# Performance work log

Hardware: AMD Instinct MI355X
Metric: run time of the kernel (lower is better)

## Reference

```python
import math
import jax, jax.numpy as jnp
import numpy as np

B, L, D_MODEL = 2, 2048, 1024
N_HEAD, HEAD_DIM = 16, 64
ATT_SCALE = 1.0  # divisor is sqrt(head_dim ** attention_scale)


def setup_inputs() -> dict:
    key = jax.random.key(0)
    ks = jax.random.split(key, 6)
    HD = N_HEAD * HEAD_DIM
    # Xavier-uniform style init for projection weights (stored as [in, out])
    def xavier(k, fan_in, fan_out):
        lim = math.sqrt(6.0 / (fan_in + fan_out))
        return jax.random.uniform(k, (fan_in, fan_out), jnp.float32, -lim, lim)
    return {
        "x":  jax.random.normal(ks[0], (B, L, D_MODEL), jnp.float32),
        "Wq": xavier(ks[1], D_MODEL, HD), "bq": jnp.zeros((HD,), jnp.float32),
        "Wk": xavier(ks[2], D_MODEL, HD), "bk": jnp.zeros((HD,), jnp.float32),
        "Wv": xavier(ks[3], D_MODEL, HD), "bv": jnp.zeros((HD,), jnp.float32),
        "Wo": xavier(ks[4], HD, D_MODEL),
        "bo": jax.random.uniform(ks[5], (D_MODEL,), jnp.float32, -1.0 / math.sqrt(HD), 1.0 / math.sqrt(HD)),
    }


def reference(x, Wq, bq, Wk, bk, Wv, bv, Wo, bo):
    b, l, _ = x.shape
    # QKV projections -> [B, L, H, Dh]
    q = (x @ Wq + bq).reshape(b, l, N_HEAD, HEAD_DIM)
    k = (x @ Wk + bk).reshape(b, l, N_HEAD, HEAD_DIM)
    v = (x @ Wv + bv).reshape(b, l, N_HEAD, HEAD_DIM)
    scale = 1.0 / math.sqrt(HEAD_DIM ** ATT_SCALE)
    # Unnormalized (no softmax) attention: (Q K^T / sqrt(Dh)) V
    scores = jnp.einsum("blhd,bmhd->bhlm", q, k) * scale  # [B,H,L,L]
    attn = jnp.einsum("bhlm,bmhd->blhd", scores, v)        # [B,L,H,Dh]
    out = attn.reshape(b, l, N_HEAD * HEAD_DIM) @ Wo + bo  # dispatcher
    return out
```

## Files before the change

kernel.cpp:

```cpp
#include <hip/hip_runtime.h>
#include <stdint.h>

#define B_ 2
#define L_ 2048
#define DM 1024
#define NH 16
#define DH 64
#define M_ (B_*L_)
#define NQKV 3072

typedef short short8 __attribute__((ext_vector_type(8)));
typedef float f32x4 __attribute__((ext_vector_type(4)));

__device__ __forceinline__ unsigned short f2b(float f) {
    union { float f; unsigned int u; } v; v.f = f;
    unsigned int u = v.u;
    return (unsigned short)((u + 0x7fffu + ((u >> 16) & 1u)) >> 16);
}

__device__ __forceinline__ void gld_lds16(const void* g, void* l) {
    __builtin_amdgcn_global_load_lds(
        (const __attribute__((address_space(1))) void*)g,
        (__attribute__((address_space(3))) void*)l, 16, 0, 0);
}

__global__ __launch_bounds__(256)
void setup_kernel(const float* __restrict__ x,
                  const float* __restrict__ Wq, const float* __restrict__ Wk,
                  const float* __restrict__ Wv, const float* __restrict__ Wo,
                  const float* __restrict__ bq, const float* __restrict__ bk,
                  const float* __restrict__ bv,
                  unsigned short* __restrict__ xb, unsigned short* __restrict__ WqkvT,
                  unsigned short* __restrict__ WoT, float* __restrict__ biasq,
                  float* __restrict__ KtV)
{
    __shared__ float tile[32][33];
    const int bid = blockIdx.x;
    const int t = threadIdx.x;

    if (bid < 2048) {
        int i = (bid * 256 + t) * 8;
        float4 a0 = *(const float4*)(x + i);
        float4 a1 = *(const float4*)(x + i + 4);
        uint4 p;
        p.x = (unsigned)f2b(a0.x) | ((unsigned)f2b(a0.y) << 16);
        p.y = (unsigned)f2b(a0.z) | ((unsigned)f2b(a0.w) << 16);
        p.z = (unsigned)f2b(a1.x) | ((unsigned)f2b(a1.y) << 16);
        p.w = (unsigned)f2b(a1.z) | ((unsigned)f2b(a1.w) << 16);
        *(uint4*)(xb + i) = p;
    } else if (bid < 2048 + 4096) {
        int wb = bid - 2048;
        int wi = wb >> 10;
        int tid = wb & 1023;
        const float* W = (wi == 0) ? Wq : (wi == 1) ? Wk : (wi == 2) ? Wv : Wo;
        unsigned short* dst = (wi < 3) ? (WqkvT + (size_t)wi * 1024 * 1024) : WoT;
        int n0 = (tid & 31) * 32, k0 = (tid >> 5) * 32;
        int r = t >> 3, c4 = (t & 7) << 2;
        float4 v = *(const float4*)(W + (size_t)(k0 + r) * DM + n0 + c4);
        tile[r][c4+0] = v.x; tile[r][c4+1] = v.y; tile[r][c4+2] = v.z; tile[r][c4+3] = v.w;
        __syncthreads();
        uint2 o;
        o.x = (unsigned)f2b(tile[c4+0][r]) | ((unsigned)f2b(tile[c4+1][r]) << 16);
        o.y = (unsigned)f2b(tile[c4+2][r]) | ((unsigned)f2b(tile[c4+3][r]) << 16);
        *(uint2*)(dst + (size_t)(n0 + r) * DM + k0 + c4) = o;
    } else if (bid < 2048 + 4096 + 12) {
        int i = (bid - 6144) * 256 + t;
        float v = (i < 1024) ? bq[i] : (i < 2048 ? bk[i - 1024] : bv[i - 2048]);
        biasq[i] = v;
    } else {
        int i = ((bid - 6156) * 256 + t) * 4;
        float4 z; z.x = z.y = z.z = z.w = 0.f;
        *(float4*)(KtV + i) = z;
    }
}

template<int BN, bool OUT_BF16, bool BATCHED_B>
__global__ __launch_bounds__(256)
void gemm_tn_kernel(const unsigned short* __restrict__ A, int lda,
                    const unsigned short* __restrict__ Bt,
                    const float* __restrict__ bias,
                    void* __restrict__ C,
                    int M, int N, int K)
{
    constexpr int BM = 128;
    constexpr int MI = (BN == 128) ? 4 : 2;
    constexpr int MJ = 4;
    __shared__ __align__(16) unsigned short As[BM * 32];
    __shared__ __align__(16) unsigned short Bs[BN * 32];

    const int t = threadIdx.x;
    const int w = t >> 6, lane = t & 63;
    const int quad = lane >> 4, l16 = lane & 15;
    const int wm = (BN == 128) ? (w >> 1) : w;
    const int wn = (BN == 128) ? (w & 1) : 0;
    const int m0 = blockIdx.y * BM, n0 = blockIdx.x * BN;

    if constexpr (BATCHED_B) Bt += (size_t)(m0 >> 11) * 1024 * 1024;

    f32x4 acc[MI][MJ];
    #pragma unroll
    for (int i = 0; i < MI; i++)
        #pragma unroll
        for (int j = 0; j < MJ; j++)
            #pragma unroll
            for (int r = 0; r < 4; r++) acc[i][j][r] = 0.f;

    const int srow = t >> 2;
    const int schunk = t & 3;

    for (int kk = 0; kk < K; kk += 32) {
        #pragma unroll
        for (int p = 0; p < 2; p++) {
            int row = p * 64 + srow;
            int g = schunk ^ ((row >> 1) & 3);
            gld_lds16(A + (size_t)(m0 + row) * lda + kk + g * 8,
                      (char*)As + p * 4096 + w * 1024);
        }
        #pragma unroll
        for (int p = 0; p < BN / 64; p++) {
            int row = p * 64 + srow;
            int g = schunk ^ ((row >> 1) & 3);
            gld_lds16(Bt + (size_t)(n0 + row) * K + kk + g * 8,
                      (char*)Bs + p * 4096 + w * 1024);
        }
        __syncthreads();

        short8 afr[MI], bfr[MJ];
        #pragma unroll
        for (int i = 0; i < MI; i++) {
            int am = wm * (MI * 16) + i * 16 + l16;
            afr[i] = *(const short8*)((const char*)As + am * 64 + ((quad ^ ((am >> 1) & 3)) << 4));
        }
        #pragma unroll
        for (int j = 0; j < MJ; j++) {
            int bn = wn * 64 + j * 16 + l16;
            bfr[j] = *(const short8*)((const char*)Bs + bn * 64 + ((quad ^ ((bn >> 1) & 3)) << 4));
        }
        #pragma unroll
        for (int i = 0; i < MI; i++)
            #pragma unroll
            for (int j = 0; j < MJ; j++)
                acc[i][j] = __builtin_amdgcn_mfma_f32_16x16x32_bf16(afr[i], bfr[j], acc[i][j], 0, 0, 0);
        __syncthreads();
    }

    #pragma unroll
    for (int j = 0; j < MJ; j++) {
        int col = n0 + wn * 64 + j * 16 + l16;
        float bv = bias[col];
        #pragma unroll
        for (int i = 0; i < MI; i++) {
            #pragma unroll
            for (int r = 0; r < 4; r++) {
                int row = m0 + wm * (MI * 16) + i * 16 + quad * 4 + r;
                float v = acc[i][j][r] + bv;
                if constexpr (OUT_BF16)
                    ((unsigned short*)C)[(size_t)row * N + col] = f2b(v);
                else
                    ((float*)C)[(size_t)row * N + col] = v;
            }
        }
    }
}


__global__ __launch_bounds__(256)
void ktv_mfma_kernel(const unsigned short* __restrict__ QKV, float* __restrict__ KtV)
{
    __shared__ __align__(16) unsigned short Ksl[64][40];
    __shared__ __align__(16) unsigned short Vsl[64][40];

    const int bh = blockIdx.x, chunk = blockIdx.y;
    const int b = bh >> 4, h = bh & 15;
    const int t = threadIdx.x;
    const int wave = t >> 6, lane = t & 63;
    const int quad = lane >> 4, l16 = lane & 15;
    const int lrow = t >> 3, c0 = (t & 7) << 3;

    f32x4 acc[4];
    #pragma unroll
    for (int i = 0; i < 4; i++)
        #pragma unroll
        for (int r = 0; r < 4; r++) acc[i][r] = 0.f;

    const size_t base0 = ((size_t)(b * L_ + chunk * 128)) * NQKV + (size_t)h * DH;
    for (int kk = 0; kk < 128; kk += 32) {
        size_t rb = base0 + (size_t)(kk + lrow) * NQKV + c0;
        uint4 kp = *(const uint4*)(QKV + rb + 1024);
        uint4 vp = *(const uint4*)(QKV + rb + 2048);
        Ksl[c0+0][lrow] = (unsigned short)(kp.x & 0xffff);
        Ksl[c0+1][lrow] = (unsigned short)(kp.x >> 16);
        Ksl[c0+2][lrow] = (unsigned short)(kp.y & 0xffff);
        Ksl[c0+3][lrow] = (unsigned short)(kp.y >> 16);
        Ksl[c0+4][lrow] = (unsigned short)(kp.z & 0xffff);
        Ksl[c0+5][lrow] = (unsigned short)(kp.z >> 16);
        Ksl[c0+6][lrow] = (unsigned short)(kp.w & 0xffff);
        Ksl[c0+7][lrow] = (unsigned short)(kp.w >> 16);
        Vsl[c0+0][lrow] = (unsigned short)(vp.x & 0xffff);
        Vsl[c0+1][lrow] = (unsigned short)(vp.x >> 16);
        Vsl[c0+2][lrow] = (unsigned short)(vp.y & 0xffff);
        Vsl[c0+3][lrow] = (unsigned short)(vp.y >> 16);
        Vsl[c0+4][lrow] = (unsigned short)(vp.z & 0xffff);
        Vsl[c0+5][lrow] = (unsigned short)(vp.z >> 16);
        Vsl[c0+6][lrow] = (unsigned short)(vp.w & 0xffff);
        Vsl[c0+7][lrow] = (unsigned short)(vp.w >> 16);
        __syncthreads();

        short8 af = *(const short8*)&Ksl[wave * 16 + l16][quad * 8];
        #pragma unroll
        for (int nt = 0; nt < 4; nt++) {
            short8 bfr = *(const short8*)&Vsl[nt * 16 + l16][quad * 8];
            acc[nt] = __builtin_amdgcn_mfma_f32_16x16x32_bf16(af, bfr, acc[nt], 0, 0, 0);
        }
        __syncthreads();
    }

    float* dst0 = KtV + (size_t)bh * 64 * 64;
    #pragma unroll
    for (int nt = 0; nt < 4; nt++) {
        int col = nt * 16 + l16;
        #pragma unroll
        for (int r = 0; r < 4; r++) {
            int row = wave * 16 + quad * 4 + r;
            atomicAdd(dst0 + row * 64 + col, acc[nt][r] * 0.125f);
        }
    }
}

__global__ __launch_bounds__(256)
void zmat_kernel(const unsigned short* __restrict__ WoT, const float* __restrict__ KtV,
                 unsigned short* __restrict__ ZT)
{
    __shared__ __align__(16) unsigned short Asl[64][72];
    __shared__ __align__(16) unsigned short Bsl[64][72];

    const int bh = blockIdx.x, nt0 = blockIdx.y;
    const int b = bh >> 4, h = bh & 15;
    const int t = threadIdx.x;
    const int wave = t >> 6, lane = t & 63;
    const int quad = lane >> 4, l16 = lane & 15;
    const int n0 = nt0 * 64;
    const int row = t >> 2, c0 = (t & 3) << 4;

    const unsigned short* ap = WoT + (size_t)(n0 + row) * DM + h * DH + c0;
    *(uint4*)&Asl[row][c0]     = *(const uint4*)ap;
    *(uint4*)&Asl[row][c0 + 8] = *(const uint4*)(ap + 8);

    const float* kp = KtV + ((size_t)bh * 64 + row) * 64 + c0;
    #pragma unroll
    for (int j = 0; j < 16; j++) Bsl[row][c0 + j] = f2b(kp[j]);
    __syncthreads();

    f32x4 acc[4];
    #pragma unroll
    for (int i = 0; i < 4; i++)
        #pragma unroll
        for (int r = 0; r < 4; r++) acc[i][r] = 0.f;

    #pragma unroll
    for (int ks = 0; ks < 2; ks++) {
        short8 af = *(const short8*)&Asl[wave * 16 + l16][ks * 32 + quad * 8];
        #pragma unroll
        for (int nt = 0; nt < 4; nt++) {
            short8 bfr = *(const short8*)&Bsl[nt * 16 + l16][ks * 32 + quad * 8];
            acc[nt] = __builtin_amdgcn_mfma_f32_16x16x32_bf16(af, bfr, acc[nt], 0, 0, 0);
        }
    }

    unsigned short* zb = ZT + (size_t)b * 1024 * 1024 + (size_t)h * DH;
    #pragma unroll
    for (int nt = 0; nt < 4; nt++) {
        int col = nt * 16 + l16;
        #pragma unroll
        for (int r = 0; r < 4; r++) {
            int zr = n0 + wave * 16 + quad * 4 + r;
            zb[(size_t)zr * 1024 + col] = f2b(acc[nt][r]);
        }
    }
}


extern "C" void kernel_launch(void* const* d_in, const int* in_sizes, int n_in,
                              void* d_out, int out_size, void* d_ws, size_t ws_size,
                              hipStream_t stream)
{
    const float* x  = (const float*)d_in[0];
    const float* Wq = (const float*)d_in[1];
    const float* bq = (const float*)d_in[2];
    const float* Wk = (const float*)d_in[3];
    const float* bk = (const float*)d_in[4];
    const float* Wv = (const float*)d_in[5];
    const float* bv = (const float*)d_in[6];
    const float* Wo = (const float*)d_in[7];
    const float* bo = (const float*)d_in[8];

    char* ws = (char*)d_ws;
    unsigned short* xb    = (unsigned short*)(ws);
    unsigned short* WqkvT = (unsigned short*)(ws + (size_t)8  * 1024 * 1024);
    unsigned short* WoT   = (unsigned short*)(ws + (size_t)14 * 1024 * 1024);
    float*          biasq = (float*)         (ws + (size_t)16 * 1024 * 1024);
    unsigned short* QKV   = (unsigned short*)(ws + (size_t)17 * 1024 * 1024);
    float*          KtV   = (float*)         (ws + (size_t)41 * 1024 * 1024);
    unsigned short* ZT    = xb;

    setup_kernel<<<6284, 256, 0, stream>>>(x, Wq, Wk, Wv, Wo, bq, bk, bv,
                                           xb, WqkvT, WoT, biasq, KtV);

    gemm_tn_kernel<128, true, false><<<dim3(NQKV / 128, M_ / 128), 256, 0, stream>>>(
        xb, DM, WqkvT, biasq, QKV, M_, NQKV, DM);

    ktv_mfma_kernel<<<dim3(B_ * NH, 16), 256, 0, stream>>>(QKV, KtV);

    zmat_kernel<<<dim3(B_ * NH, 16), 256, 0, stream>>>(WoT, KtV, ZT);

    gemm_tn_kernel<64, false, true><<<dim3(DM / 64, M_ / 128), 256, 0, stream>>>(
        QKV, NQKV, ZT, bo, d_out, M_, DM, DM);
}
```

Baseline: 164.8 us.

## Fuse K^T V reduction into QKV projection GEMM epilogue with interleaved K/V weights

Reorders the K and V weight columns so each 128-wide output tile of the QKV GEMM holds one head's K and V. The new fused kernel then computes that tile's K^T V partial product in its epilogue and atomically accumulates it, and only Q is written to global memory. This removes the separate ktv kernel and the write-then-reread of K and V, and the 1/8 scale is folded into Wk and bk. In exchange the epilogue gains extra LDS traffic, MFMA work and atomics, and the new mainloop uses direct global-to-LDS loads with a swizzled layout.

```diff
diff --git a/kernel.cpp b/kernel.cpp
--- a/kernel.cpp
+++ b/kernel.cpp
@@ -53,24 +53,215 @@
         int wi = wb >> 10;
         int tid = wb & 1023;
         const float* W = (wi == 0) ? Wq : (wi == 1) ? Wk : (wi == 2) ? Wv : Wo;
-        unsigned short* dst = (wi < 3) ? (WqkvT + (size_t)wi * 1024 * 1024) : WoT;
+        float s = (wi == 1) ? 0.125f : 1.0f;
         int n0 = (tid & 31) * 32, k0 = (tid >> 5) * 32;
         int r = t >> 3, c4 = (t & 7) << 2;
         float4 v = *(const float4*)(W + (size_t)(k0 + r) * DM + n0 + c4);
         tile[r][c4+0] = v.x; tile[r][c4+1] = v.y; tile[r][c4+2] = v.z; tile[r][c4+3] = v.w;
         __syncthreads();
         uint2 o;
-        o.x = (unsigned)f2b(tile[c4+0][r]) | ((unsigned)f2b(tile[c4+1][r]) << 16);
-        o.y = (unsigned)f2b(tile[c4+2][r]) | ((unsigned)f2b(tile[c4+3][r]) << 16);
-        *(uint2*)(dst + (size_t)(n0 + r) * DM + k0 + c4) = o;
+        o.x = (unsigned)f2b(tile[c4+0][r]*s) | ((unsigned)f2b(tile[c4+1][r]*s) << 16);
+        o.y = (unsigned)f2b(tile[c4+2][r]*s) | ((unsigned)f2b(tile[c4+3][r]*s) << 16);
+        int f = n0 + r;
+        size_t drow;
+        unsigned short* dst;
+        if (wi == 0)      { dst = WqkvT; drow = f; }
+        else if (wi == 1) { dst = WqkvT; drow = 1024 + (f >> 6) * 128 + (f & 63); }
+        else if (wi == 2) { dst = WqkvT; drow = 1024 + (f >> 6) * 128 + 64 + (f & 63); }
+        else              { dst = WoT;   drow = f; }
+        *(uint2*)(dst + drow * DM + k0 + c4) = o;
     } else if (bid < 2048 + 4096 + 12) {
-        int i = (bid - 6144) * 256 + t;
-        float v = (i < 1024) ? bq[i] : (i < 2048 ? bk[i - 1024] : bv[i - 2048]);
-        biasq[i] = v;
+        int n = (bid - 6144) * 256 + t;
+        float v;
+        if (n < 1024) v = bq[n];
+        else {
+            int kv = (n - 1024) >> 7, r = (n - 1024) & 127;
+            v = (r < 64) ? 0.125f * bk[kv * 64 + r] : bv[kv * 64 + (r - 64)];
+        }
+        biasq[n] = v;
     } else {
         int i = ((bid - 6156) * 256 + t) * 4;
         float4 z; z.x = z.y = z.z = z.w = 0.f;
         *(float4*)(KtV + i) = z;
+    }
+}
+
+__global__ __launch_bounds__(256)
+void qkv_fused_kernel(const unsigned short* __restrict__ A,
+                      const unsigned short* __restrict__ Bt,
+                      const float* __restrict__ biasq,
+                      unsigned short* __restrict__ Qb,
+                      float* __restrict__ KtV)
+{
+    __shared__ __align__(16) char smem[34816];
+    unsigned short* As = (unsigned short*)smem;
+    unsigned short* Bs = (unsigned short*)(smem + 8192);
+
+    const int t = threadIdx.x;
+    const int w = t >> 6, lane = t & 63;
+    const int quad = lane >> 4, l16 = lane & 15;
+    const int wm = w >> 1, wn = w & 1;
+    const int m0 = blockIdx.y * 128, n0 = blockIdx.x * 128;
+
+    f32x4 acc[4][4];
+    #pragma unroll
+    for (int i = 0; i < 4; i++)
+        #pragma unroll
+        for (int j = 0; j < 4; j++)
+            #pragma unroll
+            for (int r = 0; r < 4; r++) acc[i][j][r] = 0.f;
+
+    const int srow = t >> 2;
+    const int schunk = t & 3;
+
+    for (int kk = 0; kk < DM; kk += 32) {
+        #pragma unroll
+        for (int p = 0; p < 2; p++) {
+            int row = p * 64 + srow;
+            int g = schunk ^ ((row >> 1) & 3);
+            gld_lds16(A  + (size_t)(m0 + row) * DM + kk + g * 8,
+                      (char*)As + p * 4096 + w * 1024);
+            gld_lds16(Bt + (size_t)(n0 + row) * DM + kk + g * 8,
+                      (char*)Bs + p * 4096 + w * 1024);
+        }
+        __syncthreads();
+
+        short8 afr[4], bfr[4];
+        #pragma unroll
+        for (int i = 0; i < 4; i++) {
+            int am = wm * 64 + i * 16 + l16;
+            afr[i] = *(const short8*)((const char*)As + am * 64 + ((quad ^ ((am >> 1) & 3)) << 4));
+            int bn = wn * 64 + i * 16 + l16;
+            bfr[i] = *(const short8*)((const char*)Bs + bn * 64 + ((quad ^ ((bn >> 1) & 3)) << 4));
+        }
+        #pragma unroll
+        for (int i = 0; i < 4; i++)
+            #pragma unroll
+            for (int j = 0; j < 4; j++)
+                acc[i][j] = __builtin_amdgcn_mfma_f32_16x16x32_bf16(afr[i], bfr[j], acc[i][j], 0, 0, 0);
+        __syncthreads();
+    }
+
+    #pragma unroll
+    for (int j = 0; j < 4; j++) {
+        float bv = biasq[n0 + wn * 64 + j * 16 + l16];
+        #pragma unroll
+        for (int i = 0; i < 4; i++)
+            #pragma unroll
+            for (int r = 0; r < 4; r++) acc[i][j][r] += bv;
+    }
+
+    if (blockIdx.x < 8) {
+        #pragma unroll
+        for (int j = 0; j < 4; j++) {
+            int col = n0 + wn * 64 + j * 16 + l16;
+            #pragma unroll
+            for (int i = 0; i < 4; i++) {
+                #pragma unroll
+                for (int r = 0; r < 4; r++) {
+                    int row = m0 + wm * 64 + i * 16 + quad * 4 + r;
+                    Qb[(size_t)row * DM + col] = f2b(acc[i][j][r]);
+                }
+            }
+        }
+        return;
+    }
+
+    const int h  = blockIdx.x - 8;
+    const int bh = (m0 >> 11) * NH + h;
+    unsigned short (*Xt)[136] = (unsigned short (*)[136])smem;
+
+    #pragma unroll
+    for (int j = 0; j < 4; j++) {
+        int c = wn * 64 + j * 16 + l16;
+        #pragma unroll
+        for (int i = 0; i < 4; i++) {
+            int l0 = wm * 64 + i * 16 + quad * 4;
+            uint2 o;
+            o.x = (unsigned)f2b(acc[i][j][0]) | ((unsigned)f2b(acc[i][j][1]) << 16);
+            o.y = (unsigned)f2b(acc[i][j][2]) | ((unsigned)f2b(acc[i][j][3]) << 16);
+            *(uint2*)&Xt[c][l0] = o;
+        }
+    }
+    __syncthreads();
+
+    f32x4 kacc[4];
+    #pragma unroll
+    for (int j = 0; j < 4; j++)
+        #pragma unroll
+        for (int r = 0; r < 4; r++) kacc[j][r] = 0.f;
+
+    #pragma unroll
+    for (int ks = 0; ks < 4; ks++) {
+        short8 af = *(const short8*)&Xt[w * 16 + l16][ks * 32 + quad * 8];
+        #pragma unroll
+        for (int j = 0; j < 4; j++) {
+            short8 bfr = *(const short8*)&Xt[64 + j * 16 + l16][ks * 32 + quad * 8];
+            kacc[j] = __builtin_amdgcn_mfma_f32_16x16x32_bf16(af, bfr, kacc[j], 0, 0, 0);
+        }
+    }
+
+    float* dst = KtV + (size_t)bh * 64 * 64;
+    #pragma unroll
+    for (int j = 0; j < 4; j++) {
+        int col = j * 16 + l16;
+        #pragma unroll
+        for (int r = 0; r < 4; r++) {
+            int row = w * 16 + quad * 4 + r;
+            atomicAdd(dst + row * 64 + col, kacc[j][r]);
+        }
+    }
+}
+
+__global__ __launch_bounds__(256)
+void zmat_kernel(const unsigned short* __restrict__ WoT, const float* __restrict__ KtV,
+                 unsigned short* __restrict__ ZT)
+{
+    __shared__ __align__(16) unsigned short Asl[64][72];
+    __shared__ __align__(16) unsigned short Bsl[64][72];
+
+    const int bh = blockIdx.x, nt0 = blockIdx.y;
+    const int b = bh >> 4, h = bh & 15;
+    const int t = threadIdx.x;
+    const int wave = t >> 6, lane = t & 63;
+    const int quad = lane >> 4, l16 = lane & 15;
+    const int n0 = nt0 * 64;
+    const int row = t >> 2, c0 = (t & 3) << 4;
+
+    const unsigned short* ap = WoT + (size_t)(n0 + row) * DM + h * DH + c0;
+    *(uint4*)&Asl[row][c0]     = *(const uint4*)ap;
+    *(uint4*)&Asl[row][c0 + 8] = *(const uint4*)(ap + 8);
+
+    const float* kp = KtV + ((size_t)bh * 64 + row) * 64 + c0;
+    #pragma unroll
+    for (int j = 0; j < 16; j++) Bsl[row][c0 + j] = f2b(kp[j]);
+    __syncthreads();
+
+    f32x4 acc[4];
+    #pragma unroll
+    for (int i = 0; i < 4; i++)
+        #pragma unroll
+        for (int r = 0; r < 4; r++) acc[i][r] = 0.f;
+
+    #pragma unroll
+    for (int ks = 0; ks < 2; ks++) {
+        short8 af = *(const short8*)&Asl[wave * 16 + l16][ks * 32 + quad * 8];
+        #pragma unroll
+        for (int nt = 0; nt < 4; nt++) {
+            short8 bfr = *(const short8*)&Bsl[nt * 16 + l16][ks * 32 + quad * 8];
+            acc[nt] = __builtin_amdgcn_mfma_f32_16x16x32_bf16(af, bfr, acc[nt], 0, 0, 0);
+        }
+    }
+
+    unsigned short* zb = ZT + (size_t)b * 1024 * 1024 + (size_t)h * DH;
+    #pragma unroll
+    for (int nt = 0; nt < 4; nt++) {
+        int col = nt * 16 + l16;
+        #pragma unroll
+        for (int r = 0; r < 4; r++) {
+            int zr = n0 + wave * 16 + quad * 4 + r;
+            zb[(size_t)zr * 1024 + col] = f2b(acc[nt][r]);
+        }
     }
 }
 
@@ -159,122 +350,6 @@
                 else
                     ((float*)C)[(size_t)row * N + col] = v;
             }
-        }
-    }
-}
-
-
-__global__ __launch_bounds__(256)
-void ktv_mfma_kernel(const unsigned short* __restrict__ QKV, float* __restrict__ KtV)
-{
-    __shared__ __align__(16) unsigned short Ksl[64][40];
-    __shared__ __align__(16) unsigned short Vsl[64][40];
-
-    const int bh = blockIdx.x, chunk = blockIdx.y;
-    const int b = bh >> 4, h = bh & 15;
-    const int t = threadIdx.x;
-    const int wave = t >> 6, lane = t & 63;
-    const int quad = lane >> 4, l16 = lane & 15;
-    const int lrow = t >> 3, c0 = (t & 7) << 3;
-
-    f32x4 acc[4];
-    #pragma unroll
-    for (int i = 0; i < 4; i++)
-        #pragma unroll
-        for (int r = 0; r < 4; r++) acc[i][r] = 0.f;
-
-    const size_t base0 = ((size_t)(b * L_ + chunk * 128)) * NQKV + (size_t)h * DH;
-    for (int kk = 0; kk < 128; kk += 32) {
-        size_t rb = base0 + (size_t)(kk + lrow) * NQKV + c0;
-        uint4 kp = *(const uint4*)(QKV + rb + 1024);
-        uint4 vp = *(const uint4*)(QKV + rb + 2048);
-        Ksl[c0+0][lrow] = (unsigned short)(kp.x & 0xffff);
-        Ksl[c0+1][lrow] = (unsigned short)(kp.x >> 16);
-        Ksl[c0+2][lrow] = (unsigned short)(kp.y & 0xffff);
-        Ksl[c0+3][lrow] = (unsigned short)(kp.y >> 16);
-        Ksl[c0+4][lrow] = (unsigned short)(kp.z & 0xffff);
-        Ksl[c0+5][lrow] = (unsigned short)(kp.z >> 16);
-        Ksl[c0+6][lrow] = (unsigned short)(kp.w & 0xffff);
-        Ksl[c0+7][lrow] = (unsigned short)(kp.w >> 16);
-        Vsl[c0+0][lrow] = (unsigned short)(vp.x & 0xffff);
-        Vsl[c0+1][lrow] = (unsigned short)(vp.x >> 16);
-        Vsl[c0+2][lrow] = (unsigned short)(vp.y & 0xffff);
-        Vsl[c0+3][lrow] = (unsigned short)(vp.y >> 16);
-        Vsl[c0+4][lrow] = (unsigned short)(vp.z & 0xffff);
-        Vsl[c0+5][lrow] = (unsigned short)(vp.z >> 16);
-        Vsl[c0+6][lrow] = (unsigned short)(vp.w & 0xffff);
-        Vsl[c0+7][lrow] = (unsigned short)(vp.w >> 16);
-        __syncthreads();
-
-        short8 af = *(const short8*)&Ksl[wave * 16 + l16][quad * 8];
-        #pragma unroll
-        for (int nt = 0; nt < 4; nt++) {
-            short8 bfr = *(const short8*)&Vsl[nt * 16 + l16][quad * 8];
-            acc[nt] = __builtin_amdgcn_mfma_f32_16x16x32_bf16(af, bfr, acc[nt], 0, 0, 0);
-        }
-        __syncthreads();
-    }
-
-    float* dst0 = KtV + (size_t)bh * 64 * 64;
-    #pragma unroll
-    for (int nt = 0; nt < 4; nt++) {
-        int col = nt * 16 + l16;
-        #pragma unroll
-        for (int r = 0; r < 4; r++) {
-            int row = wave * 16 + quad * 4 + r;
-            atomicAdd(dst0 + row * 64 + col, acc[nt][r] * 0.125f);
-        }
-    }
-}
-
-__global__ __launch_bounds__(256)
-void zmat_kernel(const unsigned short* __restrict__ WoT, const float* __restrict__ KtV,
-                 unsigned short* __restrict__ ZT)
-{
-    __shared__ __align__(16) unsigned short Asl[64][72];
-    __shared__ __align__(16) unsigned short Bsl[64][72];
-
-    const int bh = blockIdx.x, nt0 = blockIdx.y;
-    const int b = bh >> 4, h = bh & 15;
-    const int t = threadIdx.x;
-    const int wave = t >> 6, lane = t & 63;
-    const int quad = lane >> 4, l16 = lane & 15;
-    const int n0 = nt0 * 64;
-    const int row = t >> 2, c0 = (t & 3) << 4;
-
-    const unsigned short* ap = WoT + (size_t)(n0 + row) * DM + h * DH + c0;
-    *(uint4*)&Asl[row][c0]     = *(const uint4*)ap;
-    *(uint4*)&Asl[row][c0 + 8] = *(const uint4*)(ap + 8);
-
-    const float* kp = KtV + ((size_t)bh * 64 + row) * 64 + c0;
-    #pragma unroll
-    for (int j = 0; j < 16; j++) Bsl[row][c0 + j] = f2b(kp[j]);
-    __syncthreads();
-
-    f32x4 acc[4];
-    #pragma unroll
-    for (int i = 0; i < 4; i++)
-        #pragma unroll
-        for (int r = 0; r < 4; r++) acc[i][r] = 0.f;
-
-    #pragma unroll
-    for (int ks = 0; ks < 2; ks++) {
-        short8 af = *(const short8*)&Asl[wave * 16 + l16][ks * 32 + quad * 8];
-        #pragma unroll
-        for (int nt = 0; nt < 4; nt++) {
-            short8 bfr = *(const short8*)&Bsl[nt * 16 + l16][ks * 32 + quad * 8];
-            acc[nt] = __builtin_amdgcn_mfma_f32_16x16x32_bf16(af, bfr, acc[nt], 0, 0, 0);
-        }
-    }
-
-    unsigned short* zb = ZT + (size_t)b * 1024 * 1024 + (size_t)h * DH;
-    #pragma unroll
-    for (int nt = 0; nt < 4; nt++) {
-        int col = nt * 16 + l16;
-        #pragma unroll
-        for (int r = 0; r < 4; r++) {
-            int zr = n0 + wave * 16 + quad * 4 + r;
-            zb[(size_t)zr * 1024 + col] = f2b(acc[nt][r]);
         }
     }
 }
@@ -299,20 +374,18 @@
     unsigned short* WqkvT = (unsigned short*)(ws + (size_t)8  * 1024 * 1024);
     unsigned short* WoT   = (unsigned short*)(ws + (size_t)14 * 1024 * 1024);
     float*          biasq = (float*)         (ws + (size_t)16 * 1024 * 1024);
-    unsigned short* QKV   = (unsigned short*)(ws + (size_t)17 * 1024 * 1024);
-    float*          KtV   = (float*)         (ws + (size_t)41 * 1024 * 1024);
-    unsigned short* ZT    = xb;
+    unsigned short* Qb    = (unsigned short*)(ws + (size_t)17 * 1024 * 1024);
+    unsigned short* ZT    = (unsigned short*)(ws + (size_t)25 * 1024 * 1024);
+    float*          KtV   = (float*)         (ws + (size_t)29 * 1024 * 1024);
 
     setup_kernel<<<6284, 256, 0, stream>>>(x, Wq, Wk, Wv, Wo, bq, bk, bv,
                                            xb, WqkvT, WoT, biasq, KtV);
 
-    gemm_tn_kernel<128, true, false><<<dim3(NQKV / 128, M_ / 128), 256, 0, stream>>>(
-        xb, DM, WqkvT, biasq, QKV, M_, NQKV, DM);
-
-    ktv_mfma_kernel<<<dim3(B_ * NH, 16), 256, 0, stream>>>(QKV, KtV);
+    qkv_fused_kernel<<<dim3(NQKV / 128, M_ / 128), 256, 0, stream>>>(
+        xb, WqkvT, biasq, Qb, KtV);
 
     zmat_kernel<<<dim3(B_ * NH, 16), 256, 0, stream>>>(WoT, KtV, ZT);
 
     gemm_tn_kernel<64, false, true><<<dim3(DM / 64, M_ / 128), 256, 0, stream>>>(
-        QKV, NQKV, ZT, bo, d_out, M_, DM, DM);
-}
+        Qb, DM, ZT, bo, d_out, M_, DM, DM);
+}
```

Result: faster. 151.0 us (-8.3%).
